# Performance work log

Measured on AMD Instinct MI355X. Metric: run time of the kernel, lower is better.

## Reference

```python
import jax, jax.numpy as jnp
import numpy as np

Q = 0.25          # magnetic charge q
MAX_EIGEN = 2.0   # max_eigen default

N_NODES = 1024
N_EDGES = 32768
IN_DIM = 128


def setup_inputs() -> dict:
    key = jax.random.key(0)
    k1, k2, k3, k4 = jax.random.split(key, 4)
    features = jax.random.normal(k1, (N_NODES, IN_DIM), dtype=jnp.float32)
    edges = jax.random.randint(k2, (2, N_EDGES), 0, N_NODES, dtype=jnp.int64)
    w_e1 = jax.random.normal(k3, (1, IN_DIM), dtype=jnp.float32) * (1.0 / np.sqrt(IN_DIM))
    b_e1 = jax.random.normal(k4, (1,), dtype=jnp.float32) * 0.01
    return {"features": features, "edges": edges, "w_e1": w_e1, "b_e1": b_e1, "K": 4}


def reference(features, edges, w_e1, b_e1, K):
    N = features.shape[0]
    # e1: Linear(input_dim, 1), then squeeze -> per-node scalar potential p
    p = (features @ w_e1.T + b_e1)[:, 0]                       # [N]
    u, v = edges[0], edges[1]
    val = jnp.maximum(p[u] - p[v], 0.0)                        # [M]
    w = 1.0 + val
    directed = val > 0
    # val == 0 -> self loops (u,u),(v,v); val > 0 -> (u,v),(v,u); weight 1+val each
    rows = jnp.concatenate([u, v])
    cols = jnp.concatenate([jnp.where(directed, v, u), jnp.where(directed, u, v)])
    ww = jnp.concatenate([w, w])
    A = jnp.zeros((N, N), dtype=features.dtype).at[rows, cols].add(ww)
    A = A + jnp.eye(N, dtype=features.dtype)                   # unit-weight self loops (diag_eye)

    A_sym = 0.5 * (A + A.T)
    # symmetric degree normalization (norm=True)
    d = A_sym.sum(axis=0)
    d = jnp.where(d == 0, 1.0, d) ** -0.5
    A_sym = d[:, None] * A_sym * d[None, :]

    # magnetic phase: Theta = exp(2*pi*q*i*(A - A^T))
    Theta = jnp.exp((2j * jnp.pi * Q) * (A - A.T).astype(jnp.complex64))
    I = jnp.eye(N, dtype=jnp.complex64)
    L = I - Theta * A_sym.astype(jnp.complex64)                # D=I since norm=True
    L = (2.0 / MAX_EIGEN) * L - I                              # spectral rescale

    # Chebyshev recursion: T0 = I, T1 = L, T_k = 2 L T_{k-1} - T_{k-2}
    polys = [I, L]
    for _ in range(2, K + 1):
        polys.append(2.0 * (L @ polys[-1]) - polys[-2])
    L_real = jnp.stack([t.real for t in polys])                # [K+1, N, N]
    L_img = jnp.stack([t.imag for t in polys])                 # [K+1, N, N]
    return (L_real, L_img)
```

## Files before the change

kernel.cpp:

```cpp
#include <hip/hip_runtime.h>

#define NPTS 1024
#define NN (NPTS * NPTS)
#define NEDGE 32768
#define INDIM 128

typedef __attribute__((ext_vector_type(8))) short bf16x8;
typedef __attribute__((ext_vector_type(4))) float f32x4;

__device__ inline ushort f2bf(float x) {
    union { float f; unsigned u; } v; v.f = x;
    unsigned r = (v.u + 0x7FFF + ((v.u >> 16) & 1)) >> 16;
    return (ushort)r;
}


__global__ void zeroA_p_kernel(float4* __restrict__ A4,
                               const float* __restrict__ feat,
                               const float* __restrict__ w,
                               const float* __restrict__ b,
                               float* __restrict__ p) {
    int t = threadIdx.x;
    A4[blockIdx.x * 256 + t] = make_float4(0.f, 0.f, 0.f, 0.f);
    if (blockIdx.x < 256) {
        int wid = t >> 6, lane = t & 63;
        int node = blockIdx.x * 4 + wid;
        const float* f = feat + node * INDIM;
        float s = f[lane] * w[lane] + f[lane + 64] * w[lane + 64];
#pragma unroll
        for (int off = 32; off; off >>= 1) s += __shfl_down(s, off);
        if (lane == 0) p[node] = s + b[0];
    }
}

__global__ void build_A_kernel(const int* __restrict__ eu, const int* __restrict__ ev,
                               const float* __restrict__ p, float* __restrict__ A) {
    int i = blockIdx.x * blockDim.x + threadIdx.x;
    if (i >= NEDGE) return;
    int u = eu[i], v = ev[i];
    float val = p[u] - p[v];
    if (val > 0.f) {
        float w = 1.f + val;
        atomicAdd(&A[u * NPTS + v], w);
        atomicAdd(&A[v * NPTS + u], w);
    } else {
        atomicAdd(&A[u * NPTS + u], 1.f);
        atomicAdd(&A[v * NPTS + v], 1.f);
    }
}

__global__ void row_deg_kernel(const float* __restrict__ A, float* __restrict__ dinv) {
    int wid = threadIdx.x >> 6, lane = threadIdx.x & 63;
    int row = blockIdx.x * 4 + wid;
    const float4* r4 = (const float4*)(A + (size_t)row * NPTS);
    float s = 0.f;
#pragma unroll
    for (int c = 0; c < 4; ++c) {
        float4 v = r4[c * 64 + lane];
        s += v.x + v.y + v.z + v.w;
    }
#pragma unroll
    for (int off = 32; off; off >>= 1) s += __shfl_down(s, off);
    if (lane == 0) dinv[row] = rsqrtf(s + 1.f);
}

__global__ void normalize_kernel(const float* __restrict__ A, const float* __restrict__ dinv,
                                 float* __restrict__ out, ushort* __restrict__ Mbf) {
    int idx4 = blockIdx.x * blockDim.x + threadIdx.x;
    int i = idx4 >> 8;
    int j = (idx4 & 255) * 4;
    size_t idx = (size_t)idx4 * 4;
    float di = dinv[i];
    float4 a = *(const float4*)(A + idx);
    float4 dj = *(const float4*)(dinv + j);
    float4 t0 = make_float4(0.f, 0.f, 0.f, 0.f);
    if (i == j) t0.x = 1.f;
    else if (i == j + 1) t0.y = 1.f;
    else if (i == j + 2) t0.z = 1.f;
    else if (i == j + 3) t0.w = 1.f;
    a.x += (i == j);
    a.y += (i == j + 1);
    a.z += (i == j + 2);
    a.w += (i == j + 3);
    float4 m;
    m.x = -(di * a.x * dj.x);
    m.y = -(di * a.y * dj.y);
    m.z = -(di * a.z * dj.z);
    m.w = -(di * a.w * dj.w);
    *(float4*)(out + idx) = t0;
    *(float4*)(out + NN + idx) = m;
    ushort mb[4] = {f2bf(m.x), f2bf(m.y), f2bf(m.z), f2bf(m.w)};
    *(uint2*)(Mbf + idx) = *(uint2*)mb;
}

__global__ __launch_bounds__(512) void cheb_mfma_kernel(const ushort* __restrict__ Mbf,
                                                        const ushort* __restrict__ Sbf,
                                                        float* __restrict__ out,
                                                        int phase, int zimag) {
    int mode = (phase == 0) ? 1 : (2 + blockIdx.z);

    if (phase == 1 && zimag) {
        int bid = blockIdx.z * 256 + blockIdx.y * 16 + blockIdx.x;
        float4* z = (float4*)(out + (size_t)5 * NN) + (size_t)bid * 2560 + threadIdx.x;
#pragma unroll
        for (int i = 0; i < 5; ++i) z[i * 512] = make_float4(0.f, 0.f, 0.f, 0.f);
    }

    const ushort* Ab = (mode == 2) ? Sbf : Mbf;
    const ushort* Bb = (mode == 1) ? Mbf : Sbf;

    __shared__ __align__(16) ushort sA[64][72];
    __shared__ __align__(16) ushort sB[64][72];

    int tid = threadIdx.x;
    int brow = blockIdx.y * 64, bcol = blockIdx.x * 64;

    int r = tid >> 3;
    int j0 = (tid & 7) * 8;

    int wid = tid >> 6, lane = tid & 63;
    int wr = (wid & 3) * 16, wc = (wid >> 2) * 32;
    int fr = lane & 15, g = lane >> 4;

    f32x4 acc[2] = {};
    float4 pa, pb;

    pa = *(const float4*)(Ab + (size_t)(brow + r) * NPTS + j0);
    pb = *(const float4*)(Bb + (size_t)(bcol + r) * NPTS + j0);

    const int NT = NPTS / 64;
    for (int t = 0; t < NT; ++t) {
        __syncthreads();
        *(float4*)&sA[r][j0] = pa;
        *(float4*)&sB[r][j0] = pb;
        __syncthreads();
        if (t + 1 < NT) {
            int k0 = (t + 1) * 64;
            pa = *(const float4*)(Ab + (size_t)(brow + r) * NPTS + k0 + j0);
            pb = *(const float4*)(Bb + (size_t)(bcol + r) * NPTS + k0 + j0);
        }
#pragma unroll
        for (int kc = 0; kc < 2; ++kc) {
            int kk = kc * 32 + g * 8;
            bf16x8 a0 = *(const bf16x8*)&sA[wr + fr][kk];
            bf16x8 b0 = *(const bf16x8*)&sB[wc + fr][kk];
            bf16x8 b1 = *(const bf16x8*)&sB[wc + 16 + fr][kk];
            acc[0] = __builtin_amdgcn_mfma_f32_16x16x32_bf16(a0, b0, acc[0], 0, 0, 0);
            acc[1] = __builtin_amdgcn_mfma_f32_16x16x32_bf16(a0, b1, acc[1], 0, 0, 0);
        }
    }

    float* T1 = out + (size_t)NN;
    float* T2 = out + (size_t)2 * NN;
    float* T3 = out + (size_t)3 * NN;
    float* T4 = out + (size_t)4 * NN;
    ushort* SbfW = (ushort*)Sbf;

#pragma unroll
    for (int ni = 0; ni < 2; ++ni) {
#pragma unroll
        for (int q = 0; q < 4; ++q) {
            int row = brow + wr + g * 4 + q;
            int col = bcol + wc + ni * 16 + fr;
            size_t idx = (size_t)row * NPTS + col;
            float s = acc[ni][q];
            if (mode == 1) {
                T2[idx] = 2.f * s - (row == col ? 1.f : 0.f);
                SbfW[idx] = f2bf(s);
            } else if (mode == 2) {
                T4[idx] = 8.f * s - 4.f * T2[idx] - (row == col ? 3.f : 0.f);
            } else {
                T3[idx] = 4.f * s - 3.f * T1[idx];
            }
        }
    }
}

__global__ void zero_kernel(float4* __restrict__ p, int n4) {
    int i = blockIdx.x * blockDim.x + threadIdx.x;
    if (i < n4) p[i] = make_float4(0.f, 0.f, 0.f, 0.f);
}


extern "C" void kernel_launch(void* const* d_in, const int* in_sizes, int n_in,
                              void* d_out, int out_size, void* d_ws, size_t ws_size,
                              hipStream_t stream) {
    const float* feat = (const float*)d_in[0];
    const int* edges = (const int*)d_in[1];
    const float* w_e1 = (const float*)d_in[2];
    const float* b_e1 = (const float*)d_in[3];
    float* out = (float*)d_out;

    const size_t need = (size_t)NN * 4  + (size_t)NN * 2  +
                        (size_t)NN * 2  + NPTS * 8 + 256;
    float* A;
    ushort* Mbf;
    ushort* Sbf;
    float* p;
    float* dinv;
    int use_ws = (ws_size >= need);
    if (use_ws) {
        char* w = (char*)d_ws;
        A = (float*)w;                       w += (size_t)NN * 4;
        Mbf = (ushort*)w;                    w += (size_t)NN * 2;
        Sbf = (ushort*)w;                    w += (size_t)NN * 2;
        p = (float*)w;                       w += NPTS * 4;
        dinv = (float*)w;
    } else {
        A = out + (size_t)5 * NN;
        Mbf = (ushort*)(out + (size_t)6 * NN);
        Sbf = Mbf + NN;
        p = out + (size_t)7 * NN;
        dinv = p + NPTS;
    }

    zeroA_p_kernel<<<1024, 256, 0, stream>>>((float4*)A, feat, w_e1, b_e1, p);
    build_A_kernel<<<(NEDGE + 255) / 256, 256, 0, stream>>>(edges, edges + NEDGE, p, A);
    row_deg_kernel<<<256, 256, 0, stream>>>(A, dinv);
    normalize_kernel<<<NN / 4 / 256, 256, 0, stream>>>(A, dinv, out, Mbf);

    dim3 grid1(16, 16, 1);
    cheb_mfma_kernel<<<grid1, 512, 0, stream>>>(Mbf, Sbf, out, 0, 0);
    dim3 grid2(16, 16, 2);
    cheb_mfma_kernel<<<grid2, 512, 0, stream>>>(Mbf, Sbf, out, 1, use_ws);

    if (!use_ws) {
        zero_kernel<<<(5 * NN / 4 + 255) / 256, 256, 0, stream>>>(
            (float4*)(out + (size_t)5 * NN), 5 * NN / 4);
    }
}
```

Baseline: 48.52 us.

## Split-K across wave halves and fuse T3/T4 GEMMs sharing B tile

The single Chebyshev MFMA kernel is replaced by two kernels. Each uses split-K inside the block: two groups of four waves handle alternating 64-wide K chunks, each wave computes a 32x32 sub-tile, and the partial sums are reduced through shared memory. The T3/T4 pass now runs S*S and M*S in one block over a 16x16 grid instead of using blockIdx.z. This lets both products reuse one loaded S tile, halving redundant B loads, and doubles the MFMA work per wave. In exchange the kernels use more registers and shared memory, and the T34 grid has half as many blocks.

```diff
diff --git a/kernel.cpp b/kernel.cpp
--- a/kernel.cpp
+++ b/kernel.cpp
@@ -4,6 +4,7 @@
 #define NN (NPTS * NPTS)
 #define NEDGE 32768
 #define INDIM 128
+#define PAD 72
 
 typedef __attribute__((ext_vector_type(8))) short bf16x8;
 typedef __attribute__((ext_vector_type(4))) float f32x4;
@@ -13,6 +14,8 @@
     unsigned r = (v.u + 0x7FFF + ((v.u >> 16) & 1)) >> 16;
     return (ushort)r;
 }
+
+#define MFMA(a, b, c) __builtin_amdgcn_mfma_f32_16x16x32_bf16(a, b, c, 0, 0, 0)
 
 
 __global__ void zeroA_p_kernel(float4* __restrict__ A4,
@@ -93,84 +96,193 @@
     *(uint2*)(Mbf + idx) = *(uint2*)mb;
 }
 
-__global__ __launch_bounds__(512) void cheb_mfma_kernel(const ushort* __restrict__ Mbf,
-                                                        const ushort* __restrict__ Sbf,
-                                                        float* __restrict__ out,
-                                                        int phase, int zimag) {
-    int mode = (phase == 0) ? 1 : (2 + blockIdx.z);
-
-    if (phase == 1 && zimag) {
-        int bid = blockIdx.z * 256 + blockIdx.y * 16 + blockIdx.x;
-        float4* z = (float4*)(out + (size_t)5 * NN) + (size_t)bid * 2560 + threadIdx.x;
-#pragma unroll
-        for (int i = 0; i < 5; ++i) z[i * 512] = make_float4(0.f, 0.f, 0.f, 0.f);
-    }
-
-    const ushort* Ab = (mode == 2) ? Sbf : Mbf;
-    const ushort* Bb = (mode == 1) ? Mbf : Sbf;
-
-    __shared__ __align__(16) ushort sA[64][72];
-    __shared__ __align__(16) ushort sB[64][72];
+__global__ __launch_bounds__(512) void gemm_S_kernel(const ushort* __restrict__ Mbf,
+                                                     ushort* __restrict__ Sbf,
+                                                     float* __restrict__ out) {
+    __shared__ __align__(16) ushort smem[4 * 64 * PAD];
+    ushort(*sA)[64][PAD] = (ushort(*)[64][PAD])smem;
+    ushort(*sB)[64][PAD] = (ushort(*)[64][PAD])(smem + 2 * 64 * PAD);
+    float* red = (float*)smem;
 
     int tid = threadIdx.x;
     int brow = blockIdx.y * 64, bcol = blockIdx.x * 64;
-
-    int r = tid >> 3;
-    int j0 = (tid & 7) * 8;
-
+    int r = tid >> 3, j0 = (tid & 7) * 8;
     int wid = tid >> 6, lane = tid & 63;
-    int wr = (wid & 3) * 16, wc = (wid >> 2) * 32;
+    int h = wid >> 2, w4 = wid & 3;
+    int wr = (w4 & 1) * 32, wc = (w4 >> 1) * 32;
     int fr = lane & 15, g = lane >> 4;
 
-    f32x4 acc[2] = {};
-    float4 pa, pb;
-
-    pa = *(const float4*)(Ab + (size_t)(brow + r) * NPTS + j0);
-    pb = *(const float4*)(Bb + (size_t)(bcol + r) * NPTS + j0);
-
-    const int NT = NPTS / 64;
-    for (int t = 0; t < NT; ++t) {
+    const ushort* Arow = Mbf + (size_t)(brow + r) * NPTS;
+    const ushort* Brow = Mbf + (size_t)(bcol + r) * NPTS;
+
+    f32x4 acc[2][2] = {};
+    float4 pa0 = *(const float4*)(Arow + j0);
+    float4 pa1 = *(const float4*)(Arow + 64 + j0);
+    float4 pb0 = *(const float4*)(Brow + j0);
+    float4 pb1 = *(const float4*)(Brow + 64 + j0);
+
+    for (int it = 0; it < 8; ++it) {
         __syncthreads();
-        *(float4*)&sA[r][j0] = pa;
-        *(float4*)&sB[r][j0] = pb;
+        *(float4*)&sA[0][r][j0] = pa0;
+        *(float4*)&sA[1][r][j0] = pa1;
+        *(float4*)&sB[0][r][j0] = pb0;
+        *(float4*)&sB[1][r][j0] = pb1;
         __syncthreads();
-        if (t + 1 < NT) {
-            int k0 = (t + 1) * 64;
-            pa = *(const float4*)(Ab + (size_t)(brow + r) * NPTS + k0 + j0);
-            pb = *(const float4*)(Bb + (size_t)(bcol + r) * NPTS + k0 + j0);
+        if (it < 7) {
+            int k0 = (it + 1) * 128;
+            pa0 = *(const float4*)(Arow + k0 + j0);
+            pa1 = *(const float4*)(Arow + k0 + 64 + j0);
+            pb0 = *(const float4*)(Brow + k0 + j0);
+            pb1 = *(const float4*)(Brow + k0 + 64 + j0);
         }
 #pragma unroll
         for (int kc = 0; kc < 2; ++kc) {
             int kk = kc * 32 + g * 8;
-            bf16x8 a0 = *(const bf16x8*)&sA[wr + fr][kk];
-            bf16x8 b0 = *(const bf16x8*)&sB[wc + fr][kk];
-            bf16x8 b1 = *(const bf16x8*)&sB[wc + 16 + fr][kk];
-            acc[0] = __builtin_amdgcn_mfma_f32_16x16x32_bf16(a0, b0, acc[0], 0, 0, 0);
-            acc[1] = __builtin_amdgcn_mfma_f32_16x16x32_bf16(a0, b1, acc[1], 0, 0, 0);
-        }
-    }
-
-    float* T1 = out + (size_t)NN;
-    float* T2 = out + (size_t)2 * NN;
-    float* T3 = out + (size_t)3 * NN;
-    float* T4 = out + (size_t)4 * NN;
-    ushort* SbfW = (ushort*)Sbf;
-
-#pragma unroll
-    for (int ni = 0; ni < 2; ++ni) {
+            bf16x8 a0 = *(const bf16x8*)&sA[h][wr + fr][kk];
+            bf16x8 a1 = *(const bf16x8*)&sA[h][wr + 16 + fr][kk];
+            bf16x8 b0 = *(const bf16x8*)&sB[h][wc + fr][kk];
+            bf16x8 b1 = *(const bf16x8*)&sB[h][wc + 16 + fr][kk];
+            acc[0][0] = MFMA(a0, b0, acc[0][0]);
+            acc[0][1] = MFMA(a0, b1, acc[0][1]);
+            acc[1][0] = MFMA(a1, b0, acc[1][0]);
+            acc[1][1] = MFMA(a1, b1, acc[1][1]);
+        }
+    }
+
+    __syncthreads();
+    if (h == 1) {
+#pragma unroll
+        for (int q = 0; q < 4; ++q)
+            *(f32x4*)&red[q * 1024 + (w4 * 64 + lane) * 4] = acc[q >> 1][q & 1];
+    }
+    __syncthreads();
+    if (h == 0) {
+        float* T2 = out + (size_t)2 * NN;
+#pragma unroll
+        for (int mi = 0; mi < 2; ++mi) {
+#pragma unroll
+            for (int ni = 0; ni < 2; ++ni) {
+                f32x4 o = *(f32x4*)&red[(mi * 2 + ni) * 1024 + (w4 * 64 + lane) * 4];
+#pragma unroll
+                for (int q = 0; q < 4; ++q) {
+                    int row = brow + wr + mi * 16 + g * 4 + q;
+                    int col = bcol + wc + ni * 16 + fr;
+                    size_t idx = (size_t)row * NPTS + col;
+                    float s = acc[mi][ni][q] + o[q];
+                    T2[idx] = 2.f * s - (row == col ? 1.f : 0.f);
+                    Sbf[idx] = f2bf(s);
+                }
+            }
+        }
+    }
+}
+
+__global__ __launch_bounds__(512) void gemm_T34_kernel(const ushort* __restrict__ Mbf,
+                                                       const ushort* __restrict__ Sbf,
+                                                       float* __restrict__ out,
+                                                       int zimag) {
+    if (zimag) {
+        int bid = blockIdx.y * 16 + blockIdx.x;
+        float4* z = (float4*)(out + (size_t)5 * NN) + (size_t)bid * 5120 + threadIdx.x;
+#pragma unroll
+        for (int i = 0; i < 10; ++i) z[i * 512] = make_float4(0.f, 0.f, 0.f, 0.f);
+    }
+
+    __shared__ __align__(16) ushort smem[6 * 64 * PAD];
+    ushort(*sAS)[64][PAD] = (ushort(*)[64][PAD])smem;
+    ushort(*sAM)[64][PAD] = (ushort(*)[64][PAD])(smem + 2 * 64 * PAD);
+    ushort(*sB)[64][PAD] = (ushort(*)[64][PAD])(smem + 4 * 64 * PAD);
+    float* red = (float*)smem;
+
+    int tid = threadIdx.x;
+    int brow = blockIdx.y * 64, bcol = blockIdx.x * 64;
+    int r = tid >> 3, j0 = (tid & 7) * 8;
+    int wid = tid >> 6, lane = tid & 63;
+    int h = wid >> 2, w4 = wid & 3;
+    int wr = (w4 & 1) * 32, wc = (w4 >> 1) * 32;
+    int fr = lane & 15, g = lane >> 4;
+
+    const ushort* ASrow = Sbf + (size_t)(brow + r) * NPTS;
+    const ushort* AMrow = Mbf + (size_t)(brow + r) * NPTS;
+    const ushort* Brow = Sbf + (size_t)(bcol + r) * NPTS;
+
+    f32x4 accP[2][2] = {};
+    f32x4 accR[2][2] = {};
+    float4 ps0 = *(const float4*)(ASrow + j0);
+    float4 ps1 = *(const float4*)(ASrow + 64 + j0);
+    float4 pm0 = *(const float4*)(AMrow + j0);
+    float4 pm1 = *(const float4*)(AMrow + 64 + j0);
+    float4 pb0 = *(const float4*)(Brow + j0);
+    float4 pb1 = *(const float4*)(Brow + 64 + j0);
+
+    for (int it = 0; it < 8; ++it) {
+        __syncthreads();
+        *(float4*)&sAS[0][r][j0] = ps0;
+        *(float4*)&sAS[1][r][j0] = ps1;
+        *(float4*)&sAM[0][r][j0] = pm0;
+        *(float4*)&sAM[1][r][j0] = pm1;
+        *(float4*)&sB[0][r][j0] = pb0;
+        *(float4*)&sB[1][r][j0] = pb1;
+        __syncthreads();
+        if (it < 7) {
+            int k0 = (it + 1) * 128;
+            ps0 = *(const float4*)(ASrow + k0 + j0);
+            ps1 = *(const float4*)(ASrow + k0 + 64 + j0);
+            pm0 = *(const float4*)(AMrow + k0 + j0);
+            pm1 = *(const float4*)(AMrow + k0 + 64 + j0);
+            pb0 = *(const float4*)(Brow + k0 + j0);
+            pb1 = *(const float4*)(Brow + k0 + 64 + j0);
+        }
+#pragma unroll
+        for (int kc = 0; kc < 2; ++kc) {
+            int kk = kc * 32 + g * 8;
+            bf16x8 b0 = *(const bf16x8*)&sB[h][wc + fr][kk];
+            bf16x8 b1 = *(const bf16x8*)&sB[h][wc + 16 + fr][kk];
+            bf16x8 s0 = *(const bf16x8*)&sAS[h][wr + fr][kk];
+            bf16x8 s1 = *(const bf16x8*)&sAS[h][wr + 16 + fr][kk];
+            accP[0][0] = MFMA(s0, b0, accP[0][0]);
+            accP[0][1] = MFMA(s0, b1, accP[0][1]);
+            accP[1][0] = MFMA(s1, b0, accP[1][0]);
+            accP[1][1] = MFMA(s1, b1, accP[1][1]);
+            bf16x8 m0 = *(const bf16x8*)&sAM[h][wr + fr][kk];
+            bf16x8 m1 = *(const bf16x8*)&sAM[h][wr + 16 + fr][kk];
+            accR[0][0] = MFMA(m0, b0, accR[0][0]);
+            accR[0][1] = MFMA(m0, b1, accR[0][1]);
+            accR[1][0] = MFMA(m1, b0, accR[1][0]);
+            accR[1][1] = MFMA(m1, b1, accR[1][1]);
+        }
+    }
+
+    __syncthreads();
+    if (h == 1) {
 #pragma unroll
         for (int q = 0; q < 4; ++q) {
-            int row = brow + wr + g * 4 + q;
-            int col = bcol + wc + ni * 16 + fr;
-            size_t idx = (size_t)row * NPTS + col;
-            float s = acc[ni][q];
-            if (mode == 1) {
-                T2[idx] = 2.f * s - (row == col ? 1.f : 0.f);
-                SbfW[idx] = f2bf(s);
-            } else if (mode == 2) {
-                T4[idx] = 8.f * s - 4.f * T2[idx] - (row == col ? 3.f : 0.f);
-            } else {
-                T3[idx] = 4.f * s - 3.f * T1[idx];
+            *(f32x4*)&red[q * 1024 + (w4 * 64 + lane) * 4] = accP[q >> 1][q & 1];
+            *(f32x4*)&red[4096 + q * 1024 + (w4 * 64 + lane) * 4] = accR[q >> 1][q & 1];
+        }
+    }
+    __syncthreads();
+    if (h == 0) {
+        float* T1 = out + (size_t)NN;
+        float* T2 = out + (size_t)2 * NN;
+        float* T3 = out + (size_t)3 * NN;
+        float* T4 = out + (size_t)4 * NN;
+#pragma unroll
+        for (int mi = 0; mi < 2; ++mi) {
+#pragma unroll
+            for (int ni = 0; ni < 2; ++ni) {
+                f32x4 oP = *(f32x4*)&red[(mi * 2 + ni) * 1024 + (w4 * 64 + lane) * 4];
+                f32x4 oR = *(f32x4*)&red[4096 + (mi * 2 + ni) * 1024 + (w4 * 64 + lane) * 4];
+#pragma unroll
+                for (int q = 0; q < 4; ++q) {
+                    int row = brow + wr + mi * 16 + g * 4 + q;
+                    int col = bcol + wc + ni * 16 + fr;
+                    size_t idx = (size_t)row * NPTS + col;
+                    float sp = accP[mi][ni][q] + oP[q];
+                    float sr = accR[mi][ni][q] + oR[q];
+                    T4[idx] = 8.f * sp - 4.f * T2[idx] - (row == col ? 3.f : 0.f);
+                    T3[idx] = 4.f * sr - 3.f * T1[idx];
+                }
             }
         }
     }
@@ -191,8 +303,7 @@
     const float* b_e1 = (const float*)d_in[3];
     float* out = (float*)d_out;
 
-    const size_t need = (size_t)NN * 4  + (size_t)NN * 2  +
-                        (size_t)NN * 2  + NPTS * 8 + 256;
+    const size_t need = (size_t)NN * 4 + (size_t)NN * 2 + (size_t)NN * 2 + NPTS * 8 + 256;
     float* A;
     ushort* Mbf;
     ushort* Sbf;
@@ -201,10 +312,10 @@
     int use_ws = (ws_size >= need);
     if (use_ws) {
         char* w = (char*)d_ws;
-        A = (float*)w;                       w += (size_t)NN * 4;
-        Mbf = (ushort*)w;                    w += (size_t)NN * 2;
-        Sbf = (ushort*)w;                    w += (size_t)NN * 2;
-        p = (float*)w;                       w += NPTS * 4;
+        A = (float*)w;        w += (size_t)NN * 4;
+        Mbf = (ushort*)w;     w += (size_t)NN * 2;
+        Sbf = (ushort*)w;     w += (size_t)NN * 2;
+        p = (float*)w;        w += NPTS * 4;
         dinv = (float*)w;
     } else {
         A = out + (size_t)5 * NN;
@@ -219,10 +330,9 @@
     row_deg_kernel<<<256, 256, 0, stream>>>(A, dinv);
     normalize_kernel<<<NN / 4 / 256, 256, 0, stream>>>(A, dinv, out, Mbf);
 
-    dim3 grid1(16, 16, 1);
-    cheb_mfma_kernel<<<grid1, 512, 0, stream>>>(Mbf, Sbf, out, 0, 0);
-    dim3 grid2(16, 16, 2);
-    cheb_mfma_kernel<<<grid2, 512, 0, stream>>>(Mbf, Sbf, out, 1, use_ws);
+    dim3 grid(16, 16);
+    gemm_S_kernel<<<grid, 512, 0, stream>>>(Mbf, Sbf, out);
+    gemm_T34_kernel<<<grid, 512, 0, stream>>>(Mbf, Sbf, out, use_ws);
 
     if (!use_ws) {
         zero_kernel<<<(5 * NN / 4 + 255) / 256, 256, 0, stream>>>(
```

Result: no change. 48.49 us (-0.1%).

## Compute degrees via atomics, double-buffer GEMM tiles, fuse T3/T4 GEMMs sharing B

Applied to the files above, without the earlier changes.

Drops the row-degree kernel by accumulating node degrees with atomics while A is built, then computes the inverse square roots inside the normalize kernel. Splits the Chebyshev GEMM into a dedicated S kernel and a combined T3/T4 kernel. The combined kernel loads the shared S B-tile once and runs both products over a 256-block grid instead of 512. Both GEMMs now double-buffer shared memory, so each k-step needs one barrier instead of two. The trade-offs are extra atomic traffic on the degree array, more shared memory per block, and half as many blocks in the second GEMM.

```diff
diff --git a/kernel.cpp b/kernel.cpp
--- a/kernel.cpp
+++ b/kernel.cpp
@@ -4,6 +4,7 @@
 #define NN (NPTS * NPTS)
 #define NEDGE 32768
 #define INDIM 128
+#define PAD 72
 
 typedef __attribute__((ext_vector_type(8))) short bf16x8;
 typedef __attribute__((ext_vector_type(4))) float f32x4;
@@ -14,14 +15,18 @@
     return (ushort)r;
 }
 
+#define MFMA(a, b, c) __builtin_amdgcn_mfma_f32_16x16x32_bf16(a, b, c, 0, 0, 0)
+
 
 __global__ void zeroA_p_kernel(float4* __restrict__ A4,
                                const float* __restrict__ feat,
                                const float* __restrict__ w,
                                const float* __restrict__ b,
-                               float* __restrict__ p) {
+                               float* __restrict__ p,
+                               float4* __restrict__ dd4) {
     int t = threadIdx.x;
     A4[blockIdx.x * 256 + t] = make_float4(0.f, 0.f, 0.f, 0.f);
+    if (blockIdx.x == 1024 - 1 && t < 256) dd4[t] = make_float4(0.f, 0.f, 0.f, 0.f);
     if (blockIdx.x < 256) {
         int wid = t >> 6, lane = t & 63;
         int node = blockIdx.x * 4 + wid;
@@ -34,7 +39,8 @@
 }
 
 __global__ void build_A_kernel(const int* __restrict__ eu, const int* __restrict__ ev,
-                               const float* __restrict__ p, float* __restrict__ A) {
+                               const float* __restrict__ p, float* __restrict__ A,
+                               float* __restrict__ dd) {
     int i = blockIdx.x * blockDim.x + threadIdx.x;
     if (i >= NEDGE) return;
     int u = eu[i], v = ev[i];
@@ -43,36 +49,25 @@
         float w = 1.f + val;
         atomicAdd(&A[u * NPTS + v], w);
         atomicAdd(&A[v * NPTS + u], w);
+        atomicAdd(&dd[u], w);
+        atomicAdd(&dd[v], w);
     } else {
         atomicAdd(&A[u * NPTS + u], 1.f);
         atomicAdd(&A[v * NPTS + v], 1.f);
-    }
-}
-
-__global__ void row_deg_kernel(const float* __restrict__ A, float* __restrict__ dinv) {
-    int wid = threadIdx.x >> 6, lane = threadIdx.x & 63;
-    int row = blockIdx.x * 4 + wid;
-    const float4* r4 = (const float4*)(A + (size_t)row * NPTS);
-    float s = 0.f;
-#pragma unroll
-    for (int c = 0; c < 4; ++c) {
-        float4 v = r4[c * 64 + lane];
-        s += v.x + v.y + v.z + v.w;
-    }
-#pragma unroll
-    for (int off = 32; off; off >>= 1) s += __shfl_down(s, off);
-    if (lane == 0) dinv[row] = rsqrtf(s + 1.f);
-}
-
-__global__ void normalize_kernel(const float* __restrict__ A, const float* __restrict__ dinv,
+        atomicAdd(&dd[u], 1.f);
+        atomicAdd(&dd[v], 1.f);
+    }
+}
+
+__global__ void normalize_kernel(const float* __restrict__ A, const float* __restrict__ dd,
                                  float* __restrict__ out, ushort* __restrict__ Mbf) {
     int idx4 = blockIdx.x * blockDim.x + threadIdx.x;
     int i = idx4 >> 8;
     int j = (idx4 & 255) * 4;
     size_t idx = (size_t)idx4 * 4;
-    float di = dinv[i];
+    float di = rsqrtf(dd[i] + 1.f);
     float4 a = *(const float4*)(A + idx);
-    float4 dj = *(const float4*)(dinv + j);
+    float4 d4 = *(const float4*)(dd + j);
     float4 t0 = make_float4(0.f, 0.f, 0.f, 0.f);
     if (i == j) t0.x = 1.f;
     else if (i == j + 1) t0.y = 1.f;
@@ -83,79 +78,65 @@
     a.z += (i == j + 2);
     a.w += (i == j + 3);
     float4 m;
-    m.x = -(di * a.x * dj.x);
-    m.y = -(di * a.y * dj.y);
-    m.z = -(di * a.z * dj.z);
-    m.w = -(di * a.w * dj.w);
+    m.x = -(di * a.x * rsqrtf(d4.x + 1.f));
+    m.y = -(di * a.y * rsqrtf(d4.y + 1.f));
+    m.z = -(di * a.z * rsqrtf(d4.z + 1.f));
+    m.w = -(di * a.w * rsqrtf(d4.w + 1.f));
     *(float4*)(out + idx) = t0;
     *(float4*)(out + NN + idx) = m;
     ushort mb[4] = {f2bf(m.x), f2bf(m.y), f2bf(m.z), f2bf(m.w)};
     *(uint2*)(Mbf + idx) = *(uint2*)mb;
 }
 
-__global__ __launch_bounds__(512) void cheb_mfma_kernel(const ushort* __restrict__ Mbf,
-                                                        const ushort* __restrict__ Sbf,
-                                                        float* __restrict__ out,
-                                                        int phase, int zimag) {
-    int mode = (phase == 0) ? 1 : (2 + blockIdx.z);
-
-    if (phase == 1 && zimag) {
-        int bid = blockIdx.z * 256 + blockIdx.y * 16 + blockIdx.x;
-        float4* z = (float4*)(out + (size_t)5 * NN) + (size_t)bid * 2560 + threadIdx.x;
-#pragma unroll
-        for (int i = 0; i < 5; ++i) z[i * 512] = make_float4(0.f, 0.f, 0.f, 0.f);
-    }
-
-    const ushort* Ab = (mode == 2) ? Sbf : Mbf;
-    const ushort* Bb = (mode == 1) ? Mbf : Sbf;
-
-    __shared__ __align__(16) ushort sA[64][72];
-    __shared__ __align__(16) ushort sB[64][72];
+
+__global__ __launch_bounds__(512) void gemm_S_kernel(const ushort* __restrict__ Mbf,
+                                                     ushort* __restrict__ Sbf,
+                                                     float* __restrict__ out) {
+    __shared__ __align__(16) ushort sA[2][64][PAD];
+    __shared__ __align__(16) ushort sB[2][64][PAD];
 
     int tid = threadIdx.x;
     int brow = blockIdx.y * 64, bcol = blockIdx.x * 64;
-
-    int r = tid >> 3;
-    int j0 = (tid & 7) * 8;
-
+    int r = tid >> 3, j0 = (tid & 7) * 8;
     int wid = tid >> 6, lane = tid & 63;
     int wr = (wid & 3) * 16, wc = (wid >> 2) * 32;
     int fr = lane & 15, g = lane >> 4;
 
+    const ushort* Arow = Mbf + (size_t)(brow + r) * NPTS;
+    const ushort* Brow = Mbf + (size_t)(bcol + r) * NPTS;
+
     f32x4 acc[2] = {};
-    float4 pa, pb;
-
-    pa = *(const float4*)(Ab + (size_t)(brow + r) * NPTS + j0);
-    pb = *(const float4*)(Bb + (size_t)(bcol + r) * NPTS + j0);
+    float4 pa = *(const float4*)(Arow + j0);
+    float4 pb = *(const float4*)(Brow + j0);
+    *(float4*)&sA[0][r][j0] = pa;
+    *(float4*)&sB[0][r][j0] = pb;
+    pa = *(const float4*)(Arow + 64 + j0);
+    pb = *(const float4*)(Brow + 64 + j0);
 
     const int NT = NPTS / 64;
     for (int t = 0; t < NT; ++t) {
         __syncthreads();
-        *(float4*)&sA[r][j0] = pa;
-        *(float4*)&sB[r][j0] = pb;
-        __syncthreads();
         if (t + 1 < NT) {
-            int k0 = (t + 1) * 64;
-            pa = *(const float4*)(Ab + (size_t)(brow + r) * NPTS + k0 + j0);
-            pb = *(const float4*)(Bb + (size_t)(bcol + r) * NPTS + k0 + j0);
-        }
+            *(float4*)&sA[(t + 1) & 1][r][j0] = pa;
+            *(float4*)&sB[(t + 1) & 1][r][j0] = pb;
+        }
+        if (t + 2 < NT) {
+            pa = *(const float4*)(Arow + (t + 2) * 64 + j0);
+            pb = *(const float4*)(Brow + (t + 2) * 64 + j0);
+        }
+        int cb = t & 1;
 #pragma unroll
         for (int kc = 0; kc < 2; ++kc) {
             int kk = kc * 32 + g * 8;
-            bf16x8 a0 = *(const bf16x8*)&sA[wr + fr][kk];
-            bf16x8 b0 = *(const bf16x8*)&sB[wc + fr][kk];
-            bf16x8 b1 = *(const bf16x8*)&sB[wc + 16 + fr][kk];
-            acc[0] = __builtin_amdgcn_mfma_f32_16x16x32_bf16(a0, b0, acc[0], 0, 0, 0);
-            acc[1] = __builtin_amdgcn_mfma_f32_16x16x32_bf16(a0, b1, acc[1], 0, 0, 0);
-        }
-    }
-
-    float* T1 = out + (size_t)NN;
+            bf16x8 a0 = *(const bf16x8*)&sA[cb][wr + fr][kk];
+            bf16x8 b0 = *(const bf16x8*)&sB[cb][wc + fr][kk];
+            bf16x8 b1 = *(const bf16x8*)&sB[cb][wc + 16 + fr][kk];
+            acc[0] = MFMA(a0, b0, acc[0]);
+            acc[1] = MFMA(a0, b1, acc[1]);
+        }
+    }
+
     float* T2 = out + (size_t)2 * NN;
-    float* T3 = out + (size_t)3 * NN;
-    float* T4 = out + (size_t)4 * NN;
-    ushort* SbfW = (ushort*)Sbf;
-
 #pragma unroll
     for (int ni = 0; ni < 2; ++ni) {
 #pragma unroll
@@ -164,14 +145,94 @@
             int col = bcol + wc + ni * 16 + fr;
             size_t idx = (size_t)row * NPTS + col;
             float s = acc[ni][q];
-            if (mode == 1) {
-                T2[idx] = 2.f * s - (row == col ? 1.f : 0.f);
-                SbfW[idx] = f2bf(s);
-            } else if (mode == 2) {
-                T4[idx] = 8.f * s - 4.f * T2[idx] - (row == col ? 3.f : 0.f);
-            } else {
-                T3[idx] = 4.f * s - 3.f * T1[idx];
-            }
+            T2[idx] = 2.f * s - (row == col ? 1.f : 0.f);
+            Sbf[idx] = f2bf(s);
+        }
+    }
+}
+
+__global__ __launch_bounds__(512) void gemm_T34_kernel(const ushort* __restrict__ Mbf,
+                                                       const ushort* __restrict__ Sbf,
+                                                       float* __restrict__ out,
+                                                       int zimag) {
+    if (zimag) {
+        int bid = blockIdx.y * 16 + blockIdx.x;
+        float4* z = (float4*)(out + (size_t)5 * NN) + (size_t)bid * 5120 + threadIdx.x;
+#pragma unroll
+        for (int i = 0; i < 10; ++i) z[i * 512] = make_float4(0.f, 0.f, 0.f, 0.f);
+    }
+
+    __shared__ __align__(16) ushort sAS[2][64][PAD];
+    __shared__ __align__(16) ushort sAM[2][64][PAD];
+    __shared__ __align__(16) ushort sB[2][64][PAD];
+
+    int tid = threadIdx.x;
+    int brow = blockIdx.y * 64, bcol = blockIdx.x * 64;
+    int r = tid >> 3, j0 = (tid & 7) * 8;
+    int wid = tid >> 6, lane = tid & 63;
+    int wr = (wid & 3) * 16, wc = (wid >> 2) * 32;
+    int fr = lane & 15, g = lane >> 4;
+
+    const ushort* ASrow = Sbf + (size_t)(brow + r) * NPTS;
+    const ushort* AMrow = Mbf + (size_t)(brow + r) * NPTS;
+    const ushort* Brow = Sbf + (size_t)(bcol + r) * NPTS;
+
+    f32x4 accP[2] = {};
+    f32x4 accR[2] = {};
+    float4 ps = *(const float4*)(ASrow + j0);
+    float4 pm = *(const float4*)(AMrow + j0);
+    float4 pb = *(const float4*)(Brow + j0);
+    *(float4*)&sAS[0][r][j0] = ps;
+    *(float4*)&sAM[0][r][j0] = pm;
+    *(float4*)&sB[0][r][j0] = pb;
+    ps = *(const float4*)(ASrow + 64 + j0);
+    pm = *(const float4*)(AMrow + 64 + j0);
+    pb = *(const float4*)(Brow + 64 + j0);
+
+    const int NT = NPTS / 64;
+    for (int t = 0; t < NT; ++t) {
+        __syncthreads();
+        if (t + 1 < NT) {
+            *(float4*)&sAS[(t + 1) & 1][r][j0] = ps;
+            *(float4*)&sAM[(t + 1) & 1][r][j0] = pm;
+            *(float4*)&sB[(t + 1) & 1][r][j0] = pb;
+        }
+        if (t + 2 < NT) {
+            int k0 = (t + 2) * 64;
+            ps = *(const float4*)(ASrow + k0 + j0);
+            pm = *(const float4*)(AMrow + k0 + j0);
+            pb = *(const float4*)(Brow + k0 + j0);
+        }
+        int cb = t & 1;
+#pragma unroll
+        for (int kc = 0; kc < 2; ++kc) {
+            int kk = kc * 32 + g * 8;
+            bf16x8 b0 = *(const bf16x8*)&sB[cb][wc + fr][kk];
+            bf16x8 b1 = *(const bf16x8*)&sB[cb][wc + 16 + fr][kk];
+            bf16x8 s0 = *(const bf16x8*)&sAS[cb][wr + fr][kk];
+            bf16x8 m0 = *(const bf16x8*)&sAM[cb][wr + fr][kk];
+            accP[0] = MFMA(s0, b0, accP[0]);
+            accP[1] = MFMA(s0, b1, accP[1]);
+            accR[0] = MFMA(m0, b0, accR[0]);
+            accR[1] = MFMA(m0, b1, accR[1]);
+        }
+    }
+
+    float* T1 = out + (size_t)NN;
+    float* T2 = out + (size_t)2 * NN;
+    float* T3 = out + (size_t)3 * NN;
+    float* T4 = out + (size_t)4 * NN;
+#pragma unroll
+    for (int ni = 0; ni < 2; ++ni) {
+#pragma unroll
+        for (int q = 0; q < 4; ++q) {
+            int row = brow + wr + g * 4 + q;
+            int col = bcol + wc + ni * 16 + fr;
+            size_t idx = (size_t)row * NPTS + col;
+            float sp = accP[ni][q];
+            float sr = accR[ni][q];
+            T4[idx] = 8.f * sp - 4.f * T2[idx] - (row == col ? 3.f : 0.f);
+            T3[idx] = 4.f * sr - 3.f * T1[idx];
         }
     }
 }
@@ -191,38 +252,35 @@
     const float* b_e1 = (const float*)d_in[3];
     float* out = (float*)d_out;
 
-    const size_t need = (size_t)NN * 4  + (size_t)NN * 2  +
-                        (size_t)NN * 2  + NPTS * 8 + 256;
+    const size_t need = (size_t)NN * 4 + (size_t)NN * 2 + (size_t)NN * 2 + NPTS * 8 + 256;
     float* A;
     ushort* Mbf;
     ushort* Sbf;
     float* p;
-    float* dinv;
+    float* dd;
     int use_ws = (ws_size >= need);
     if (use_ws) {
         char* w = (char*)d_ws;
-        A = (float*)w;                       w += (size_t)NN * 4;
-        Mbf = (ushort*)w;                    w += (size_t)NN * 2;
-        Sbf = (ushort*)w;                    w += (size_t)NN * 2;
-        p = (float*)w;                       w += NPTS * 4;
-        dinv = (float*)w;
+        A = (float*)w;        w += (size_t)NN * 4;
+        Mbf = (ushort*)w;     w += (size_t)NN * 2;
+        Sbf = (ushort*)w;     w += (size_t)NN * 2;
+        p = (float*)w;        w += NPTS * 4;
+        dd = (float*)w;
     } else {
         A = out + (size_t)5 * NN;
         Mbf = (ushort*)(out + (size_t)6 * NN);
         Sbf = Mbf + NN;
         p = out + (size_t)7 * NN;
-        dinv = p + NPTS;
-    }
-
-    zeroA_p_kernel<<<1024, 256, 0, stream>>>((float4*)A, feat, w_e1, b_e1, p);
-    build_A_kernel<<<(NEDGE + 255) / 256, 256, 0, stream>>>(edges, edges + NEDGE, p, A);
-    row_deg_kernel<<<256, 256, 0, stream>>>(A, dinv);
-    normalize_kernel<<<NN / 4 / 256, 256, 0, stream>>>(A, dinv, out, Mbf);
-
-    dim3 grid1(16, 16, 1);
-    cheb_mfma_kernel<<<grid1, 512, 0, stream>>>(Mbf, Sbf, out, 0, 0);
-    dim3 grid2(16, 16, 2);
-    cheb_mfma_kernel<<<grid2, 512, 0, stream>>>(Mbf, Sbf, out, 1, use_ws);
+        dd = p + NPTS;
+    }
+
+    zeroA_p_kernel<<<1024, 256, 0, stream>>>((float4*)A, feat, w_e1, b_e1, p, (float4*)dd);
+    build_A_kernel<<<(NEDGE + 255) / 256, 256, 0, stream>>>(edges, edges + NEDGE, p, A, dd);
+    normalize_kernel<<<NN / 4 / 256, 256, 0, stream>>>(A, dd, out, Mbf);
+
+    dim3 grid(16, 16);
+    gemm_S_kernel<<<grid, 512, 0, stream>>>(Mbf, Sbf, out);
+    gemm_T34_kernel<<<grid, 512, 0, stream>>>(Mbf, Sbf, out, use_ws);
 
     if (!use_ws) {
         zero_kernel<<<(5 * NN / 4 + 255) / 256, 256, 0, stream>>>(
```

New measurement: 59.11 us. 21.8% more time.
